# Optimization experiments

Measured on AMD Instinct MI355X. Metric: run time of the kernel, lower is better.

Reference implementation:

```python
import jax, jax.numpy as jnp
import numpy as np

NUM_HEADS = 16
HEAD_DIM = 64  # embed_dim // num_heads
ROPE_BASE = 10000.0


def _apply_rope(x):
    # x: (B, H, S, D) -- standard rotate-half RoPE over the head dim
    B, H, S, D = x.shape
    inv_freq = 1.0 / (ROPE_BASE ** (jnp.arange(0, D, 2, dtype=jnp.float32) / D))  # (D/2,)
    ang = jnp.arange(S, dtype=jnp.float32)[:, None] * inv_freq[None, :]           # (S, D/2)
    emb = jnp.concatenate([ang, ang], axis=-1)                                     # (S, D)
    cos = jnp.cos(emb)[None, None].astype(x.dtype)
    sin = jnp.sin(emb)[None, None].astype(x.dtype)
    x1, x2 = x[..., : D // 2], x[..., D // 2 :]
    rot = jnp.concatenate([-x2, x1], axis=-1)
    return x * cos + rot * sin


def setup_inputs() -> dict:
    key = jax.random.key(0)
    ks = jax.random.split(key, 9)
    B, S, E, R = 2, 2048, 1024, 256
    s = 0.02
    return {
        "x": jax.random.normal(ks[0], (B, S, E), jnp.float32),
        "wq_down": jax.random.normal(ks[1], (R, E), jnp.float32) * s,
        "wk_rope": jax.random.normal(ks[2], (R, E), jnp.float32) * s,
        "wkv_down": jax.random.normal(ks[3], (R, E), jnp.float32) * s,
        "wq_rope": jax.random.normal(ks[4], (E, R), jnp.float32) * s,
        "wq_up": jax.random.normal(ks[5], (E, R), jnp.float32) * s,
        "wk_up": jax.random.normal(ks[6], (E, R), jnp.float32) * s,
        "wv_up": jax.random.normal(ks[7], (E, R), jnp.float32) * s,
        "wo": jax.random.normal(ks[8], (E, E), jnp.float32) * s,
    }


def _heads(t, B, S):
    # (B, S, E) -> (B, H, S, D)
    return t.reshape(B, S, NUM_HEADS, HEAD_DIM).transpose(0, 2, 1, 3)


def reference(x, wq_down, wk_rope, wkv_down, wq_rope, wq_up, wk_up, wv_up, wo):
    B, S, E = x.shape
    # low-rank query path
    q_lat = x @ wq_down.T                         # (B, S, R)
    q_r = _apply_rope(_heads(q_lat @ wq_rope.T, B, S))
    q_n = _heads(q_lat @ wq_up.T, B, S)
    q = jnp.concatenate([q_r, q_n], axis=-1)      # (B, H, S, 2D)
    # key rope path (separate latent)
    k_r = _apply_rope(_heads((x @ wk_rope.T) @ wk_up.T, B, S))
    # shared kv latent
    kv = x @ wkv_down.T                           # (B, S, R)
    k_n = _heads(kv @ wk_up.T, B, S)
    k = jnp.concatenate([k_r, k_n], axis=-1)      # (B, H, S, 2D)
    v = _heads(kv @ wv_up.T, B, S)                # (B, H, S, D)
    # causal SDPA, scale = 1/sqrt(q_dim) = 1/sqrt(2*HEAD_DIM)
    scale = 1.0 / jnp.sqrt(jnp.array(2 * HEAD_DIM, dtype=x.dtype))
    scores = jnp.einsum("bhqd,bhkd->bhqk", q, k) * scale
    mask = jnp.tril(jnp.ones((S, S), dtype=bool))
    scores = jnp.where(mask[None, None], scores, jnp.finfo(scores.dtype).min)
    attn = jax.nn.softmax(scores, axis=-1)
    y = jnp.einsum("bhqk,bhkd->bhqd", attn, v)    # (B, H, S, D)
    y = y.transpose(0, 2, 1, 3).reshape(B, S, E)
    return y @ wo.T
```

## Files before the change

kernel.cpp:

```cpp
#include <hip/hip_runtime.h>
#include <hip/hip_bf16.h>
#include <math.h>


typedef __attribute__((ext_vector_type(8))) short  short8;
typedef __attribute__((ext_vector_type(4))) float  floatx4;

static __device__ __forceinline__ unsigned short f2bf(float f) {
    __hip_bfloat16 h = __float2bfloat16(f);
    return *reinterpret_cast<unsigned short*>(&h);
}

#define GLL16(gp, lp) __builtin_amdgcn_global_load_lds( \
    (const __attribute__((address_space(1))) void*)(gp), \
    (__attribute__((address_space(3))) void*)(lp), 16, 0, 0)

struct CastDesc { const float* src; unsigned short* dst; int n4; };
struct CastArgs { CastDesc d[9]; };

__global__ __launch_bounds__(256) void cast_bf16_multi(CastArgs a)
{
    CastDesc dd = a.d[blockIdx.y];
    const int stride = gridDim.x * 256;
    for (int i = blockIdx.x * 256 + threadIdx.x; i < dd.n4; i += stride) {
        float4 v = ((const float4*)dd.src)[i];
        ushort4 o = make_ushort4(f2bf(v.x), f2bf(v.y), f2bf(v.z), f2bf(v.w));
        ((ushort4*)dd.dst)[i] = o;
    }
}

template<int MODE>
__global__ __launch_bounds__(128) void gemm64(
    const unsigned short* __restrict__ A, int lda,
    const unsigned short* __restrict__ B0,
    const unsigned short* __restrict__ B1,
    const unsigned short* __restrict__ B2, int nspan, int ldb,
    void* __restrict__ Cout, int ldc, int K, float oscale)
{
    __shared__ __align__(16) unsigned short As[64 * 32];
    __shared__ __align__(16) unsigned short Bs[64 * 32];

    const int t    = threadIdx.x;
    const int w    = t >> 6;
    const int lane = t & 63;
    const int li   = lane & 15;
    const int quad = lane >> 4;
    const int m0   = blockIdx.y * 64;
    const int n0   = blockIdx.x * 64;

    const unsigned short* Bp = (n0 < nspan) ? B0 : ((n0 < 2 * nspan) ? B1 : B2);
    const int nb0 = n0 % nspan;

    const unsigned short* ga = A  + (size_t)(m0  + w * 32 + (lane >> 2)) * lda + (lane & 3) * 8;
    const unsigned short* gb = Bp + (size_t)(nb0 + w * 32 + (lane >> 2)) * ldb + (lane & 3) * 8;
    unsigned short* lA0 = &As[(w * 32) * 32];
    unsigned short* lA1 = &As[(w * 32 + 16) * 32];
    unsigned short* lB0 = &Bs[(w * 32) * 32];
    unsigned short* lB1 = &Bs[(w * 32 + 16) * 32];

    floatx4 acc[2][4];
    #pragma unroll
    for (int i = 0; i < 2; ++i)
        #pragma unroll
        for (int j = 0; j < 4; ++j)
            acc[i][j] = (floatx4){0.f, 0.f, 0.f, 0.f};

    for (int k0 = 0; k0 < K; k0 += 32) {
        __syncthreads();
        GLL16(ga + k0,            lA0);
        GLL16(ga + 16 * lda + k0, lA1);
        GLL16(gb + k0,            lB0);
        GLL16(gb + 16 * ldb + k0, lB1);
        __syncthreads();

        short8 af[2], bfr[4];
        #pragma unroll
        for (int mb = 0; mb < 2; ++mb)
            af[mb] = *(const short8*)&As[(w * 32 + mb * 16 + li) * 32 + quad * 8];
        #pragma unroll
        for (int nb = 0; nb < 4; ++nb)
            bfr[nb] = *(const short8*)&Bs[(nb * 16 + li) * 32 + quad * 8];
        #pragma unroll
        for (int mb = 0; mb < 2; ++mb)
            #pragma unroll
            for (int nb = 0; nb < 4; ++nb)
                acc[mb][nb] = __builtin_amdgcn_mfma_f32_16x16x32_bf16(
                    af[mb], bfr[nb], acc[mb][nb], 0, 0, 0);
    }

    if (MODE == 0) {
        float* C = (float*)Cout;
        #pragma unroll
        for (int mb = 0; mb < 2; ++mb)
            #pragma unroll
            for (int nb = 0; nb < 4; ++nb) {
                const int m = m0 + w * 32 + mb * 16 + quad * 4;
                const int n = n0 + nb * 16 + li;
                #pragma unroll
                for (int r = 0; r < 4; ++r)
                    C[(size_t)(m + r) * ldc + n] = acc[mb][nb][r] * oscale;
            }
    } else {
        unsigned short* C = (unsigned short*)Cout;
        #pragma unroll
        for (int mb = 0; mb < 2; ++mb)
            #pragma unroll
            for (int nb = 0; nb < 4; ++nb) {
                const int m = m0 + w * 32 + mb * 16 + quad * 4;
                const int n = n0 + nb * 16 + li;
                #pragma unroll
                for (int r = 0; r < 4; ++r)
                    C[(size_t)(m + r) * ldc + n] = f2bf(acc[mb][nb][r] * oscale);
            }
    }
}

__global__ __launch_bounds__(256) void gemm_qkv(
    const unsigned short* __restrict__ lat,
    const unsigned short* __restrict__ wqr, const unsigned short* __restrict__ wqu,
    const unsigned short* __restrict__ wku, const unsigned short* __restrict__ wvu,
    unsigned short* __restrict__ Qp, unsigned short* __restrict__ Kp,
    unsigned short* __restrict__ Vt, float qscale)
{
    __shared__ __align__(16) unsigned short As[128 * 32];
    __shared__ __align__(16) unsigned short Bs[128 * 32];

    const int t    = threadIdx.x;
    const int w    = t >> 6;
    const int lane = t & 63;
    const int li   = lane & 15;
    const int quad = lane >> 4;
    const int wr   = w >> 1, wc = w & 1;
    const int m0   = blockIdx.y * 128;
    const int n0   = blockIdx.x * 128;

    const unsigned short* Ap;
    const unsigned short* Bp;
    int nloc, seg;
    if (n0 < 1024)      { seg = 0; Ap = lat;       Bp = wqr; nloc = n0; }
    else if (n0 < 2048) { seg = 1; Ap = lat;       Bp = wqu; nloc = n0 - 1024; }
    else if (n0 < 3072) { seg = 2; Ap = lat + 256; Bp = wku; nloc = n0 - 2048; }
    else if (n0 < 4096) { seg = 3; Ap = lat + 512; Bp = wku; nloc = n0 - 3072; }
    else                { seg = 4; Ap = lat + 512; Bp = wvu; nloc = n0 - 4096; }
    const float oscale = (seg <= 1) ? qscale : 1.0f;

    const unsigned short* ga = Ap + (size_t)(m0   + w * 32 + (lane >> 2)) * 768 + (lane & 3) * 8;
    const unsigned short* gb = Bp + (size_t)(nloc + w * 32 + (lane >> 2)) * 256 + (lane & 3) * 8;
    unsigned short* lA0 = &As[(w * 32) * 32];
    unsigned short* lA1 = &As[(w * 32 + 16) * 32];
    unsigned short* lB0 = &Bs[(w * 32) * 32];
    unsigned short* lB1 = &Bs[(w * 32 + 16) * 32];

    floatx4 acc[4][4];
    #pragma unroll
    for (int i = 0; i < 4; ++i)
        #pragma unroll
        for (int j = 0; j < 4; ++j)
            acc[i][j] = (floatx4){0.f, 0.f, 0.f, 0.f};

    for (int k0 = 0; k0 < 256; k0 += 32) {
        __syncthreads();
        GLL16(ga + k0,            lA0);
        GLL16(ga + 16 * 768 + k0, lA1);
        GLL16(gb + k0,            lB0);
        GLL16(gb + 16 * 256 + k0, lB1);
        __syncthreads();

        short8 af[4], bfr[4];
        #pragma unroll
        for (int mb = 0; mb < 4; ++mb)
            af[mb] = *(const short8*)&As[(wr * 64 + mb * 16 + li) * 32 + quad * 8];
        #pragma unroll
        for (int nb = 0; nb < 4; ++nb)
            bfr[nb] = *(const short8*)&Bs[(wc * 64 + nb * 16 + li) * 32 + quad * 8];
        #pragma unroll
        for (int mb = 0; mb < 4; ++mb)
            #pragma unroll
            for (int nb = 0; nb < 4; ++nb)
                acc[mb][nb] = __builtin_amdgcn_mfma_f32_16x16x32_bf16(
                    af[mb], bfr[nb], acc[mb][nb], 0, 0, 0);
    }

    const int h = ((nloc + wc * 64) >> 6) & 15;

    if (seg == 0) {
        float invf[2];
        #pragma unroll
        for (int nb = 0; nb < 2; ++nb)
            invf[nb] = exp2f((float)(nb * 16 + li) * -0.4152410118609203f);
        #pragma unroll
        for (int mb = 0; mb < 4; ++mb) {
            const int m = m0 + wr * 64 + mb * 16 + quad * 4;
            const int b = m >> 11, s = m & 2047;
            #pragma unroll
            for (int nb = 0; nb < 2; ++nb) {
                const int dd = nb * 16 + li;
                size_t o = ((size_t)(b * 16 + h) * 2048 + s) * 128 + dd;
                #pragma unroll
                for (int r = 0; r < 4; ++r) {
                    float ang = (float)(s + r) * invf[nb];
                    float sn, cs;
                    sincosf(ang, &sn, &cs);
                    float x1 = acc[mb][nb][r], x2 = acc[mb][nb + 2][r];
                    Qp[o + (size_t)r * 128]      = f2bf((x1 * cs - x2 * sn) * oscale);
                    Qp[o + (size_t)r * 128 + 32] = f2bf((x2 * cs + x1 * sn) * oscale);
                }
            }
        }
    } else if (seg == 1) {
        #pragma unroll
        for (int mb = 0; mb < 4; ++mb)
            #pragma unroll
            for (int nb = 0; nb < 4; ++nb) {
                const int m = m0 + wr * 64 + mb * 16 + quad * 4;
                const int n = nloc + wc * 64 + nb * 16 + li;
                const int dn = n & 63;
                const int b = m >> 11, s = m & 2047;
                size_t o = ((size_t)(b * 16 + h) * 2048 + s) * 128 + 64 + dn;
                #pragma unroll
                for (int r = 0; r < 4; ++r)
                    Qp[o + (size_t)r * 128] = f2bf(acc[mb][nb][r] * oscale);
            }
    } else if (seg == 2) {
        float invf[2];
        #pragma unroll
        for (int nb = 0; nb < 2; ++nb)
            invf[nb] = exp2f((float)(nb * 16 + li) * -0.4152410118609203f);
        #pragma unroll
        for (int mb = 0; mb < 4; ++mb) {
            const int m = m0 + wr * 64 + mb * 16 + quad * 4;
            const int b = m >> 11, sba = m & 2047;
            #pragma unroll
            for (int nb = 0; nb < 2; ++nb) {
                const int dd = nb * 16 + li;
                const int d2 = dd + 32;
                #pragma unroll
                for (int r = 0; r < 4; ++r) {
                    const int s = sba + r;
                    float ang = (float)s * invf[nb];
                    float sn, cs;
                    sincosf(ang, &sn, &cs);
                    float x1 = acc[mb][nb][r], x2 = acc[mb][nb + 2][r];
                    size_t base = (size_t)(b * 16 + h) * 262144
                                + (size_t)(s >> 5) * 4096 + (size_t)(s & 31) * 8;
                    Kp[base + (dd >> 3) * 256 + (dd & 7)] = f2bf(x1 * cs - x2 * sn);
                    Kp[base + (d2 >> 3) * 256 + (d2 & 7)] = f2bf(x2 * cs + x1 * sn);
                }
            }
        }
    } else if (seg == 3) {
        #pragma unroll
        for (int mb = 0; mb < 4; ++mb)
            #pragma unroll
            for (int nb = 0; nb < 4; ++nb) {
                const int m = m0 + wr * 64 + mb * 16 + quad * 4;
                const int n = nloc + wc * 64 + nb * 16 + li;
                const int d = 64 + (n & 63);
                const int b = m >> 11, sba = m & 2047;
                #pragma unroll
                for (int r = 0; r < 4; ++r) {
                    const int s = sba + r;
                    size_t o = (size_t)(b * 16 + h) * 262144 + (size_t)(s >> 5) * 4096
                             + (size_t)(d >> 3) * 256 + (size_t)(s & 31) * 8 + (d & 7);
                    Kp[o] = f2bf(acc[mb][nb][r]);
                }
            }
    } else {
        #pragma unroll
        for (int mb = 0; mb < 4; ++mb)
            #pragma unroll
            for (int nb = 0; nb < 4; ++nb) {
                const int m = m0 + wr * 64 + mb * 16 + quad * 4;
                const int n = nloc + wc * 64 + nb * 16 + li;
                const int dn = n & 63;
                const int b = m >> 11, s = m & 2047;
                ushort4 st = make_ushort4(f2bf(acc[mb][nb][0]), f2bf(acc[mb][nb][1]),
                                          f2bf(acc[mb][nb][2]), f2bf(acc[mb][nb][3]));
                size_t o = (size_t)(b * 16 + h) * 131072 + (size_t)(s >> 5) * 2048
                         + (size_t)((s & 31) >> 3) * 512 + (size_t)dn * 8 + (s & 7);
                *(ushort4*)&Vt[o] = st;
            }
    }
}

__global__ __launch_bounds__(256, 4) void attn_mfma(
    const unsigned short* __restrict__ Qp, const unsigned short* __restrict__ Kp,
    const unsigned short* __restrict__ Vt, unsigned short* __restrict__ y)
{
    __shared__ __align__(16) unsigned short Ks[2][4096];
    __shared__ __align__(16) unsigned short PT[4][640];

    const int t    = threadIdx.x;
    const int w    = t >> 6;
    const int lane = t & 63;
    const int li   = lane & 15;
    const int quad = lane >> 4;

    const int blk = blockIdx.x;
    const int xcd = blk & 7;
    const int g   = blk >> 3;
    const int bh  = xcd + 8 * (g & 3);
    const int qt  = 31 - (g >> 2);
    const int b   = bh >> 4, h = bh & 15;

    const unsigned short* Kb = Kp + (size_t)bh * 262144;
    const unsigned short* Vb = Vt + (size_t)bh * 131072;
    const int qbase  = qt * 64 + w * 16;
    const int NKT    = 2 * qt + 2;
    const int lastkt = (qbase + 15) >> 5;

    const unsigned short* Qb = Qp + ((size_t)bh * 2048 + qbase) * 128;
    short8 qf[4];
    #pragma unroll
    for (int kb = 0; kb < 4; ++kb)
        qf[kb] = *(const short8*)(Qb + (size_t)li * 128 + kb * 32 + quad * 8);

    short8 onesf;
    #pragma unroll
    for (int j = 0; j < 8; ++j) onesf[j] = (short)0x3F80;

    floatx4 o0 = {0.f,0.f,0.f,0.f}, o1 = {0.f,0.f,0.f,0.f};
    floatx4 o2 = {0.f,0.f,0.f,0.f}, o3 = {0.f,0.f,0.f,0.f};
    floatx4 ol = {0.f,0.f,0.f,0.f};

    unsigned short* Pw = &PT[w][0];

    auto stageK = [&](int kt, int buf) {
        const unsigned short* gk = Kb + (size_t)kt * 4096 + w * 1024 + (size_t)lane * 8;
        GLL16(gk,       &Ks[buf][w * 1024]);
        GLL16(gk + 512, &Ks[buf][w * 1024 + 512]);
    };
    auto loadV = [&](int kt, short8 vf[4]) {
        const unsigned short* gv = Vb + (size_t)kt * 2048 + quad * 512 + li * 8;
        #pragma unroll
        for (int nb = 0; nb < 4; ++nb)
            vf[nb] = *(const short8*)(gv + nb * 128);
    };
    auto compute = [&](int kt, int buf, short8 vf[4], bool maskTile) {
        const int kbase = kt * 32;
        floatx4 s0 = {0.f,0.f,0.f,0.f}, s1 = {0.f,0.f,0.f,0.f};
        #pragma unroll
        for (int kb = 0; kb < 4; ++kb) {
            short8 k0 = *(const short8*)&Ks[buf][(kb * 4 + quad) * 256 + li * 8];
            short8 k1 = *(const short8*)&Ks[buf][(kb * 4 + quad) * 256 + (16 + li) * 8];
            s0 = __builtin_amdgcn_mfma_f32_16x16x32_bf16(qf[kb], k0, s0, 0, 0, 0);
            s1 = __builtin_amdgcn_mfma_f32_16x16x32_bf16(qf[kb], k1, s1, 0, 0, 0);
        }
        #pragma unroll
        for (int r = 0; r < 4; ++r) {
            const int i = quad * 4 + r;
            unsigned int u0 = __float_as_uint(__expf(s0[r])) >> 16;
            unsigned int u1 = __float_as_uint(__expf(s1[r])) >> 16;
            if (maskTile) {
                const int qrow = qbase + i;
                u0 = (kbase + li      <= qrow) ? u0 : 0u;
                u1 = (kbase + 16 + li <= qrow) ? u1 : 0u;
            }
            Pw[i * 40 + li]      = (unsigned short)u0;
            Pw[i * 40 + 16 + li] = (unsigned short)u1;
        }
        short8 pf = *(const short8*)&Pw[li * 40 + quad * 8];

        ol = __builtin_amdgcn_mfma_f32_16x16x32_bf16(pf, onesf, ol, 0, 0, 0);
        o0 = __builtin_amdgcn_mfma_f32_16x16x32_bf16(pf, vf[0], o0, 0, 0, 0);
        o1 = __builtin_amdgcn_mfma_f32_16x16x32_bf16(pf, vf[1], o1, 0, 0, 0);
        o2 = __builtin_amdgcn_mfma_f32_16x16x32_bf16(pf, vf[2], o2, 0, 0, 0);
        o3 = __builtin_amdgcn_mfma_f32_16x16x32_bf16(pf, vf[3], o3, 0, 0, 0);
    };

    short8 vfa[4], vfb[4];
    stageK(0, 0);
    loadV(0, vfa);

    int kt = 0;
    while (true) {
        __syncthreads();
        if (kt + 1 < NKT) {
            stageK(kt + 1, 1);
            if (kt + 1 <= lastkt) loadV(kt + 1, vfb);
        }
        if (kt <= lastkt) compute(kt, 0, vfa, kt == lastkt);
        ++kt; if (kt == NKT) break;
        __syncthreads();
        if (kt + 1 < NKT) {
            stageK(kt + 1, 0);
            if (kt + 1 <= lastkt) loadV(kt + 1, vfa);
        }
        if (kt <= lastkt) compute(kt, 1, vfb, kt == lastkt);
        ++kt; if (kt == NKT) break;
    }

    unsigned short* yb2 = y + ((size_t)b * 2048 + qbase + quad * 4) * 1024 + h * 64 + li;
    #pragma unroll
    for (int r = 0; r < 4; ++r) {
        const float linv = 1.0f / ol[r];
        yb2[(size_t)r * 1024 + 0]  = f2bf(o0[r] * linv);
        yb2[(size_t)r * 1024 + 16] = f2bf(o1[r] * linv);
        yb2[(size_t)r * 1024 + 32] = f2bf(o2[r] * linv);
        yb2[(size_t)r * 1024 + 48] = f2bf(o3[r] * linv);
    }
}

extern "C" void kernel_launch(void* const* d_in, const int* in_sizes, int n_in,
                              void* d_out, int out_size, void* d_ws, size_t ws_size,
                              hipStream_t stream)
{
    const float* x        = (const float*)d_in[0];
    const float* wq_down  = (const float*)d_in[1];
    const float* wk_rope  = (const float*)d_in[2];
    const float* wkv_down = (const float*)d_in[3];
    const float* wq_rope  = (const float*)d_in[4];
    const float* wq_up    = (const float*)d_in[5];
    const float* wk_up    = (const float*)d_in[6];
    const float* wv_up    = (const float*)d_in[7];
    const float* wo       = (const float*)d_in[8];
    float* out = (float*)d_out;

    char* wsb = (char*)d_ws;
    const size_t MB = 1u << 20;
    unsigned short* xb   = (unsigned short*)(wsb + 0 * MB);
    unsigned short* lat  = (unsigned short*)(wsb + 8 * MB);
    unsigned short* Qp   = (unsigned short*)(wsb + 14 * MB);
    unsigned short* Kp   = (unsigned short*)(wsb + 30 * MB);
    unsigned short* Vt   = (unsigned short*)(wsb + 46 * MB);
    unsigned short* yb   = (unsigned short*)(wsb + 54 * MB);
    unsigned short* wqd_b = (unsigned short*)(wsb + 62 * MB);
    unsigned short* wkr_b = (unsigned short*)(wsb + 63 * MB);
    unsigned short* wkd_b = (unsigned short*)(wsb + 64 * MB);
    unsigned short* wqr_b = (unsigned short*)(wsb + 65 * MB);
    unsigned short* wqu_b = (unsigned short*)(wsb + 66 * MB);
    unsigned short* wku_b = (unsigned short*)(wsb + 67 * MB);
    unsigned short* wvu_b = (unsigned short*)(wsb + 68 * MB);
    unsigned short* wo_b  = (unsigned short*)(wsb + 69 * MB);

    const float scale = 0.08838834764831845f;
    const int BIG = 1 << 30;
    dim3 blk(256);

    CastArgs ca;
    ca.d[0] = { x,        xb,    4194304 / 4 };
    ca.d[1] = { wq_down,  wqd_b,  262144 / 4 };
    ca.d[2] = { wk_rope,  wkr_b,  262144 / 4 };
    ca.d[3] = { wkv_down, wkd_b,  262144 / 4 };
    ca.d[4] = { wq_rope,  wqr_b,  262144 / 4 };
    ca.d[5] = { wq_up,    wqu_b,  262144 / 4 };
    ca.d[6] = { wk_up,    wku_b,  262144 / 4 };
    ca.d[7] = { wv_up,    wvu_b,  262144 / 4 };
    ca.d[8] = { wo,       wo_b,  1048576 / 4 };
    cast_bf16_multi<<<dim3(128, 9), blk, 0, stream>>>(ca);

    gemm64<3><<<dim3(12, 64), dim3(128), 0, stream>>>(
        xb, 1024, wqd_b, wkr_b, wkd_b, 256, 1024, lat, 768, 1024, 1.f);

    gemm_qkv<<<dim3(40, 32), blk, 0, stream>>>(
        lat, wqr_b, wqu_b, wku_b, wvu_b, Qp, Kp, Vt, scale);

    attn_mfma<<<dim3(1024), blk, 0, stream>>>(Qp, Kp, Vt, yb);

    gemm64<0><<<dim3(16, 64), dim3(128), 0, stream>>>(
        yb, 1024, wo_b, wo_b, wo_b, BIG, 1024, out, 1024, 1024, 1.f);
}
```

Measured before the change: 210.6 us.

## Balance causal attention work by pairing query tiles and splitting long rows

Rebalances the causal attention grid so each block does roughly equal work. One variant runs a short early query tile plus the first half of a long late tile, and the other runs the second half of that late tile. Partial unnormalized outputs and row sums for the split tiles go to fp32 workspace buffers. A new combine kernel adds the two halves and normalizes them. This aims to remove tail imbalance from blocks with very different KV lengths, at the cost of extra fp32 global traffic and one extra kernel launch.

```diff
diff --git a/kernel.cpp b/kernel.cpp
--- a/kernel.cpp
+++ b/kernel.cpp
@@ -285,7 +285,9 @@
 
 __global__ __launch_bounds__(256, 4) void attn_mfma(
     const unsigned short* __restrict__ Qp, const unsigned short* __restrict__ Kp,
-    const unsigned short* __restrict__ Vt, unsigned short* __restrict__ y)
+    const unsigned short* __restrict__ Vt, unsigned short* __restrict__ y,
+    float* __restrict__ O0, float* __restrict__ O1,
+    float* __restrict__ l0, float* __restrict__ l1)
 {
     __shared__ __align__(16) unsigned short Ks[2][4096];
     __shared__ __align__(16) unsigned short PT[4][640];
@@ -300,105 +302,158 @@
     const int xcd = blk & 7;
     const int g   = blk >> 3;
     const int bh  = xcd + 8 * (g & 3);
-    const int qt  = 31 - (g >> 2);
+    const int u   = g >> 2;
+    const int p   = u >> 1;
+    const int var = u & 1;
     const int b   = bh >> 4, h = bh & 15;
 
     const unsigned short* Kb = Kp + (size_t)bh * 262144;
     const unsigned short* Vb = Vt + (size_t)bh * 131072;
-    const int qbase  = qt * 64 + w * 16;
-    const int NKT    = 2 * qt + 2;
-    const int lastkt = (qbase + 15) >> 5;
-
-    const unsigned short* Qb = Qp + ((size_t)bh * 2048 + qbase) * 128;
-    short8 qf[4];
-    #pragma unroll
-    for (int kb = 0; kb < 4; ++kb)
-        qf[kb] = *(const short8*)(Qb + (size_t)li * 128 + kb * 32 + quad * 8);
 
     short8 onesf;
     #pragma unroll
     for (int j = 0; j < 8; ++j) onesf[j] = (short)0x3F80;
 
-    floatx4 o0 = {0.f,0.f,0.f,0.f}, o1 = {0.f,0.f,0.f,0.f};
-    floatx4 o2 = {0.f,0.f,0.f,0.f}, o3 = {0.f,0.f,0.f,0.f};
-    floatx4 ol = {0.f,0.f,0.f,0.f};
-
     unsigned short* Pw = &PT[w][0];
 
-    auto stageK = [&](int kt, int buf) {
-        const unsigned short* gk = Kb + (size_t)kt * 4096 + w * 1024 + (size_t)lane * 8;
-        GLL16(gk,       &Ks[buf][w * 1024]);
-        GLL16(gk + 512, &Ks[buf][w * 1024 + 512]);
+    auto run_seg = [&](int qt, int lo, int hi, int mode) {
+        const int qbase  = qt * 64 + w * 16;
+        const int lastkt = 2 * qt + (w >> 1);
+
+        const unsigned short* Qb = Qp + ((size_t)bh * 2048 + qbase) * 128;
+        short8 qf[4];
+        #pragma unroll
+        for (int kb = 0; kb < 4; ++kb)
+            qf[kb] = *(const short8*)(Qb + (size_t)li * 128 + kb * 32 + quad * 8);
+
+        floatx4 o0 = {0.f,0.f,0.f,0.f}, o1 = {0.f,0.f,0.f,0.f};
+        floatx4 o2 = {0.f,0.f,0.f,0.f}, o3 = {0.f,0.f,0.f,0.f};
+        floatx4 ol = {0.f,0.f,0.f,0.f};
+
+        auto stageK = [&](int kt, int buf) {
+            const unsigned short* gk = Kb + (size_t)kt * 4096 + w * 1024 + (size_t)lane * 8;
+            GLL16(gk,       &Ks[buf][w * 1024]);
+            GLL16(gk + 512, &Ks[buf][w * 1024 + 512]);
+        };
+        auto loadV = [&](int kt, short8 vf[4]) {
+            const unsigned short* gv = Vb + (size_t)kt * 2048 + quad * 512 + li * 8;
+            #pragma unroll
+            for (int nb = 0; nb < 4; ++nb)
+                vf[nb] = *(const short8*)(gv + nb * 128);
+        };
+        auto compute = [&](int kt, int buf, short8 vf[4], bool maskTile) {
+            const int kbase = kt * 32;
+            floatx4 s0 = {0.f,0.f,0.f,0.f}, s1 = {0.f,0.f,0.f,0.f};
+            #pragma unroll
+            for (int kb = 0; kb < 4; ++kb) {
+                short8 k0 = *(const short8*)&Ks[buf][(kb * 4 + quad) * 256 + li * 8];
+                short8 k1 = *(const short8*)&Ks[buf][(kb * 4 + quad) * 256 + (16 + li) * 8];
+                s0 = __builtin_amdgcn_mfma_f32_16x16x32_bf16(qf[kb], k0, s0, 0, 0, 0);
+                s1 = __builtin_amdgcn_mfma_f32_16x16x32_bf16(qf[kb], k1, s1, 0, 0, 0);
+            }
+            #pragma unroll
+            for (int r = 0; r < 4; ++r) {
+                const int i = quad * 4 + r;
+                unsigned int u0 = __float_as_uint(__expf(s0[r])) >> 16;
+                unsigned int u1 = __float_as_uint(__expf(s1[r])) >> 16;
+                if (maskTile) {
+                    const int qrow = qbase + i;
+                    u0 = (kbase + li      <= qrow) ? u0 : 0u;
+                    u1 = (kbase + 16 + li <= qrow) ? u1 : 0u;
+                }
+                Pw[i * 40 + li]      = (unsigned short)u0;
+                Pw[i * 40 + 16 + li] = (unsigned short)u1;
+            }
+            short8 pf = *(const short8*)&Pw[li * 40 + quad * 8];
+
+            ol = __builtin_amdgcn_mfma_f32_16x16x32_bf16(pf, onesf, ol, 0, 0, 0);
+            o0 = __builtin_amdgcn_mfma_f32_16x16x32_bf16(pf, vf[0], o0, 0, 0, 0);
+            o1 = __builtin_amdgcn_mfma_f32_16x16x32_bf16(pf, vf[1], o1, 0, 0, 0);
+            o2 = __builtin_amdgcn_mfma_f32_16x16x32_bf16(pf, vf[2], o2, 0, 0, 0);
+            o3 = __builtin_amdgcn_mfma_f32_16x16x32_bf16(pf, vf[3], o3, 0, 0, 0);
+        };
+
+        short8 vfa[4], vfb[4];
+        __syncthreads();
+        stageK(lo, 0);
+        if (lo <= lastkt) loadV(lo, vfa);
+
+        int kt = lo;
+        while (true) {
+            __syncthreads();
+            if (kt + 1 < hi) {
+                stageK(kt + 1, 1);
+                if (kt + 1 <= lastkt) loadV(kt + 1, vfb);
+            }
+            if (kt <= lastkt) compute(kt, 0, vfa, kt == lastkt);
+            ++kt; if (kt == hi) break;
+            __syncthreads();
+            if (kt + 1 < hi) {
+                stageK(kt + 1, 0);
+                if (kt + 1 <= lastkt) loadV(kt + 1, vfa);
+            }
+            if (kt <= lastkt) compute(kt, 1, vfb, kt == lastkt);
+            ++kt; if (kt == hi) break;
+        }
+
+        if (mode == 0) {
+            unsigned short* yb2 = y + ((size_t)b * 2048 + qbase + quad * 4) * 1024 + h * 64 + li;
+            #pragma unroll
+            for (int r = 0; r < 4; ++r) {
+                const float linv = 1.0f / ol[r];
+                yb2[(size_t)r * 1024 + 0]  = f2bf(o0[r] * linv);
+                yb2[(size_t)r * 1024 + 16] = f2bf(o1[r] * linv);
+                yb2[(size_t)r * 1024 + 32] = f2bf(o2[r] * linv);
+                yb2[(size_t)r * 1024 + 48] = f2bf(o3[r] * linv);
+            }
+        } else {
+            float* Op = (mode == 1) ? O0 : O1;
+            float* lp = (mode == 1) ? l0 : l1;
+            const int rowL = qbase - 1024 + quad * 4;
+            float* ob = Op + ((size_t)bh * 1024 + rowL) * 64 + li;
+            #pragma unroll
+            for (int r = 0; r < 4; ++r) {
+                ob[(size_t)r * 64 + 0]  = o0[r];
+                ob[(size_t)r * 64 + 16] = o1[r];
+                ob[(size_t)r * 64 + 32] = o2[r];
+                ob[(size_t)r * 64 + 48] = o3[r];
+            }
+            if (li == 0) {
+                #pragma unroll
+                for (int r = 0; r < 4; ++r)
+                    lp[bh * 1024 + rowL + r] = ol[r];
+            }
+        }
     };
-    auto loadV = [&](int kt, short8 vf[4]) {
-        const unsigned short* gv = Vb + (size_t)kt * 2048 + quad * 512 + li * 8;
-        #pragma unroll
-        for (int nb = 0; nb < 4; ++nb)
-            vf[nb] = *(const short8*)(gv + nb * 128);
-    };
-    auto compute = [&](int kt, int buf, short8 vf[4], bool maskTile) {
-        const int kbase = kt * 32;
-        floatx4 s0 = {0.f,0.f,0.f,0.f}, s1 = {0.f,0.f,0.f,0.f};
-        #pragma unroll
-        for (int kb = 0; kb < 4; ++kb) {
-            short8 k0 = *(const short8*)&Ks[buf][(kb * 4 + quad) * 256 + li * 8];
-            short8 k1 = *(const short8*)&Ks[buf][(kb * 4 + quad) * 256 + (16 + li) * 8];
-            s0 = __builtin_amdgcn_mfma_f32_16x16x32_bf16(qf[kb], k0, s0, 0, 0, 0);
-            s1 = __builtin_amdgcn_mfma_f32_16x16x32_bf16(qf[kb], k1, s1, 0, 0, 0);
-        }
-        #pragma unroll
-        for (int r = 0; r < 4; ++r) {
-            const int i = quad * 4 + r;
-            unsigned int u0 = __float_as_uint(__expf(s0[r])) >> 16;
-            unsigned int u1 = __float_as_uint(__expf(s1[r])) >> 16;
-            if (maskTile) {
-                const int qrow = qbase + i;
-                u0 = (kbase + li      <= qrow) ? u0 : 0u;
-                u1 = (kbase + 16 + li <= qrow) ? u1 : 0u;
-            }
-            Pw[i * 40 + li]      = (unsigned short)u0;
-            Pw[i * 40 + 16 + li] = (unsigned short)u1;
-        }
-        short8 pf = *(const short8*)&Pw[li * 40 + quad * 8];
-
-        ol = __builtin_amdgcn_mfma_f32_16x16x32_bf16(pf, onesf, ol, 0, 0, 0);
-        o0 = __builtin_amdgcn_mfma_f32_16x16x32_bf16(pf, vf[0], o0, 0, 0, 0);
-        o1 = __builtin_amdgcn_mfma_f32_16x16x32_bf16(pf, vf[1], o1, 0, 0, 0);
-        o2 = __builtin_amdgcn_mfma_f32_16x16x32_bf16(pf, vf[2], o2, 0, 0, 0);
-        o3 = __builtin_amdgcn_mfma_f32_16x16x32_bf16(pf, vf[3], o3, 0, 0, 0);
-    };
-
-    short8 vfa[4], vfb[4];
-    stageK(0, 0);
-    loadV(0, vfa);
-
-    int kt = 0;
-    while (true) {
-        __syncthreads();
-        if (kt + 1 < NKT) {
-            stageK(kt + 1, 1);
-            if (kt + 1 <= lastkt) loadV(kt + 1, vfb);
-        }
-        if (kt <= lastkt) compute(kt, 0, vfa, kt == lastkt);
-        ++kt; if (kt == NKT) break;
-        __syncthreads();
-        if (kt + 1 < NKT) {
-            stageK(kt + 1, 0);
-            if (kt + 1 <= lastkt) loadV(kt + 1, vfa);
-        }
-        if (kt <= lastkt) compute(kt, 1, vfb, kt == lastkt);
-        ++kt; if (kt == NKT) break;
+
+    if (var == 0) {
+        run_seg(p, 0, 2 * p + 2, 0);
+        run_seg(31 - p, 0, 31 - 2 * p, 1);
+    } else {
+        run_seg(31 - p, 31 - 2 * p, 64 - 2 * p, 2);
     }
-
-    unsigned short* yb2 = y + ((size_t)b * 2048 + qbase + quad * 4) * 1024 + h * 64 + li;
-    #pragma unroll
-    for (int r = 0; r < 4; ++r) {
-        const float linv = 1.0f / ol[r];
-        yb2[(size_t)r * 1024 + 0]  = f2bf(o0[r] * linv);
-        yb2[(size_t)r * 1024 + 16] = f2bf(o1[r] * linv);
-        yb2[(size_t)r * 1024 + 32] = f2bf(o2[r] * linv);
-        yb2[(size_t)r * 1024 + 48] = f2bf(o3[r] * linv);
-    }
+}
+
+__global__ __launch_bounds__(256) void attn_combine(
+    const float* __restrict__ O0, const float* __restrict__ O1,
+    const float* __restrict__ l0, const float* __restrict__ l1,
+    unsigned short* __restrict__ y)
+{
+    const int idx = blockIdx.x * 256 + threadIdx.x;
+    const int c4  = idx & 15;
+    const int row = (idx >> 4) & 1023;
+    const int bh  = idx >> 14;
+    const int b   = bh >> 4, h = bh & 15;
+
+    const size_t o = ((size_t)bh * 1024 + row) * 64 + c4 * 4;
+    float4 a  = *(const float4*)&O0[o];
+    float4 c  = *(const float4*)&O1[o];
+    const float linv = 1.0f / (l0[bh * 1024 + row] + l1[bh * 1024 + row]);
+
+    ushort4 st = make_ushort4(f2bf((a.x + c.x) * linv), f2bf((a.y + c.y) * linv),
+                              f2bf((a.z + c.z) * linv), f2bf((a.w + c.w) * linv));
+    const size_t yo = ((size_t)b * 2048 + 1024 + row) * 1024 + h * 64 + c4 * 4;
+    *(ushort4*)&y[yo] = st;
 }
 
 extern "C" void kernel_launch(void* const* d_in, const int* in_sizes, int n_in,
@@ -432,6 +487,10 @@
     unsigned short* wku_b = (unsigned short*)(wsb + 67 * MB);
     unsigned short* wvu_b = (unsigned short*)(wsb + 68 * MB);
     unsigned short* wo_b  = (unsigned short*)(wsb + 69 * MB);
+    float* O0p = (float*)(wsb + 71 * MB);
+    float* O1p = (float*)(wsb + 79 * MB);
+    float* l0p = (float*)(wsb + 87 * MB);
+    float* l1p = (float*)(wsb + 87 * MB + (1u << 17));
 
     const float scale = 0.08838834764831845f;
     const int BIG = 1 << 30;
@@ -455,7 +514,8 @@
     gemm_qkv<<<dim3(40, 32), blk, 0, stream>>>(
         lat, wqr_b, wqu_b, wku_b, wvu_b, Qp, Kp, Vt, scale);
 
-    attn_mfma<<<dim3(1024), blk, 0, stream>>>(Qp, Kp, Vt, yb);
+    attn_mfma<<<dim3(1024), blk, 0, stream>>>(Qp, Kp, Vt, yb, O0p, O1p, l0p, l1p);
+    attn_combine<<<dim3(2048), blk, 0, stream>>>(O0p, O1p, l0p, l1p, yb);
 
     gemm64<0><<<dim3(16, 64), dim3(128), 0, stream>>>(
         yb, 1024, wo_b, wo_b, wo_b, BIG, 1024, out, 1024, 1024, 1.f);
```

Result: no change. 211.4 us (+0.4%).
